# Kernel tuning notes

Measured on AMD Instinct MI355X. Metric: run time of the kernel, lower is better.

Reference implementation:

```python
import jax, jax.numpy as jnp
import numpy as np

V = 50000      # vocab size
FEAT = 300     # glove dim
HID = 512      # num_hidden
C = 20         # class_num (GAT feature width)
L = 2          # num_layers
NH = 4         # num_heads
K = 3          # diffusion hops
ALPHA = 0.1    # teleport prob
N = 76800      # total nodes in batched graph
E = 1250000    # total edges
B = 512        # number of graphs (docs)
SLOPE = 0.2    # leaky relu slope (DGL GAT default)


def setup_inputs() -> dict:
    key = jax.random.key(0)
    ks = jax.random.split(key, 12)
    node_ids = jax.random.randint(ks[0], (N,), 0, V)
    edge_src = jax.random.randint(ks[1], (E,), 0, N)
    edge_dst = jax.random.randint(ks[2], (E,), 0, N)
    graph_ids = jnp.sort(jax.random.randint(ks[3], (N,), 0, B))
    emb = jax.random.uniform(ks[4], (V, FEAT), minval=-0.1, maxval=0.1, dtype=jnp.float32)
    W1 = jax.random.normal(ks[5], (FEAT, HID), dtype=jnp.float32) / np.sqrt(FEAT)
    b1 = jnp.zeros((HID,), jnp.float32)
    W2 = jax.random.normal(ks[6], (HID, C), dtype=jnp.float32) / np.sqrt(HID)
    b2 = jnp.zeros((C,), jnp.float32)
    gat_W = jax.random.normal(ks[7], (L, NH, C, C), dtype=jnp.float32) / np.sqrt(C)
    gat_asrc = jax.random.normal(ks[8], (L, NH, C), dtype=jnp.float32) * 0.1
    gat_adst = jax.random.normal(ks[9], (L, NH, C), dtype=jnp.float32) * 0.1
    ws_W = jax.random.normal(ks[10], (C, 1), dtype=jnp.float32) / np.sqrt(C)
    ws_b = jnp.zeros((1,), jnp.float32)
    return {"node_ids": node_ids, "edge_src": edge_src, "edge_dst": edge_dst,
            "graph_ids": graph_ids, "emb": emb, "W1": W1, "b1": b1, "W2": W2,
            "b2": b2, "gat_W": gat_W, "gat_asrc": gat_asrc, "gat_adst": gat_adst,
            "ws_W": ws_W, "ws_b": ws_b}


def _segment_softmax(e, dst, n):
    # e: [NH, E] edge scores; softmax over edges sharing the same destination node
    seg_max = jax.vmap(lambda v: jax.ops.segment_max(v, dst, num_segments=n))(e)
    seg_max = jnp.where(jnp.isfinite(seg_max), seg_max, 0.0)
    ex = jnp.exp(e - seg_max[:, dst])
    denom = jax.vmap(lambda v: jax.ops.segment_sum(v, dst, num_segments=n))(ex)
    return ex / (denom[:, dst] + 1e-9)


def _forward(node_ids, edge_src, edge_dst, graph_ids, emb, W1, b1, W2, b2,
             gat_W, gat_asrc, gat_adst, ws_W, ws_b):
    x = jnp.take(emb, node_ids, axis=0)              # [N, FEAT] embedding lookup
    x = jax.nn.relu(x @ W1 + b1)                     # [N, HID]
    h = x @ W2 + b2                                  # [N, C]
    for l in range(L):
        z = jnp.einsum('nc,hcd->hnd', h, gat_W[l])   # [NH, N, C]
        es = jnp.einsum('hnd,hd->hn', z, gat_asrc[l])
        ed = jnp.einsum('hnd,hd->hn', z, gat_adst[l])
        e = jax.nn.leaky_relu(es[:, edge_src] + ed[:, edge_dst], SLOPE)  # [NH, E]
        att = _segment_softmax(e, edge_dst, N)       # [NH, E]
        # attention diffusion: H <- (1-alpha) * A_att @ H + alpha * H0
        H0 = z
        Hc = z
        for _ in range(K):
            msg = att[:, :, None] * Hc[:, edge_src, :]                     # [NH, E, C]
            agg = jax.vmap(lambda m: jax.ops.segment_sum(m, edge_dst, num_segments=N))(msg)
            Hc = (1.0 - ALPHA) * agg + ALPHA * H0
        h = Hc.mean(axis=0)                          # merge='mean' over heads
        if l < L - 1:
            h = jax.nn.elu(h)
    gate = jax.nn.sigmoid(h @ ws_W + ws_b)           # [N, 1] WeightAndSum gate
    return jax.ops.segment_sum(h * gate, graph_ids, num_segments=B)  # [B, C]


def reference(node_ids, edge_src, edge_dst, graph_ids, emb, W1, b1, W2, b2,
              gat_W, gat_asrc, gat_adst, ws_W, ws_b):
    return _forward(node_ids, edge_src, edge_dst, graph_ids, emb, W1, b1, W2, b2,
                    gat_W, gat_asrc, gat_adst, ws_W, ws_b)
```

## Files before the change

### kernel.cpp

```cpp
#include <hip/hip_runtime.h>
#include <hip/hip_bf16.h>
#include <hip/hip_fp16.h>
#include <math.h>

#define VOCAB 50000
#define FEAT 300
#define KPAD 320
#define HID 512
#define C 20
#define NL 2
#define NH 4
#define KHOP 3
#define ALPHA 0.1f
#define NNODE 76800
#define NEDGE 1250000
#define NB 512
#define SLOPE 0.2f

#define NBKT 300
#define BKTCAP 5120
#define NSLOT (NBKT * BKTCAP)
#define EPB 5120
#define NEBLK ((NEDGE + EPB - 1) / EPB)

#define BM 32
#define VPAD 50048
#define SX_STRIDE 520
#define HP 24

typedef float f32x4 __attribute__((ext_vector_type(4)));
typedef short bf16x8 __attribute__((ext_vector_type(8)));

__device__ inline unsigned short f2b(float x) {
  __hip_bfloat16 h = __float2bfloat16(x);
  return *reinterpret_cast<unsigned short*>(&h);
}

union U48 {
  uint4 u[3];
  __half2 h[12];
};
__device__ inline U48 ldrow16(const __half* p) {
  U48 r;
  const uint4* q = (const uint4*)p;
  r.u[0] = q[0]; r.u[1] = q[1]; r.u[2] = q[2];
  return r;
}

#define H2SWZ(v, pat) ({ union { __half2 h; int i; } _u; _u.h = (v);          \
                         _u.i = __builtin_amdgcn_ds_swizzle(_u.i, (pat));     \
                         _u.h; })
#define FSWZ(x, pat) __int_as_float(                                          \
    __builtin_amdgcn_ds_swizzle(__float_as_int(x), (pat)))
#define SLOTRED_H2(v) do {                                                    \
    v = __hadd2(v, H2SWZ(v, 0x101F));                                         \
    v = __hadd2(v, H2SWZ(v, 0x201F));                                         \
    v = __hadd2(v, H2SWZ(v, 0x401F)); } while (0)

__global__ void k_cvt_w1(const float* __restrict__ W1, ushort* __restrict__ W1t)
{
  int idx = blockIdx.x * 256 + threadIdx.x;
  int kc = idx >> 12;
  int rem = idx & 4095;
  int col = rem >> 3;
  int j = rem & 7;
  int k = kc * 8 + j;
  W1t[idx] = (k < FEAT) ? f2b(W1[(size_t)k * HID + col]) : (ushort)0;
}

__global__ void k_prep_coef(const float* __restrict__ gatW0,
                            const float* __restrict__ as0,
                            const float* __restrict__ ad0,
                            const float* __restrict__ b2,
                            float* __restrict__ coef, float* __restrict__ bb)
{
  int col = threadIdx.x;
  if (col >= 96) return;
  float cf[C];
  if (col < 80) {
    int hd = col / C, d = col - hd * C;
#pragma unroll
    for (int j = 0; j < C; j++) cf[j] = gatW0[(hd * C + j) * C + d];
  } else if (col < 88) {
    int hd = col - 80;
#pragma unroll
    for (int j = 0; j < C; j++) {
      float s = 0.f;
#pragma unroll
      for (int d = 0; d < C; d++) s += gatW0[(hd * C + j) * C + d] * as0[hd * C + d];
      cf[j] = s;
    }
  } else {
    int hd = col - 88;
#pragma unroll
    for (int j = 0; j < C; j++) {
      float s = 0.f;
#pragma unroll
      for (int d = 0; d < C; d++) s += gatW0[(hd * C + j) * C + d] * ad0[hd * C + d];
      cf[j] = s;
    }
  }
  float bbv = 0.f;
#pragma unroll
  for (int j = 0; j < C; j++) { coef[col * C + j] = cf[j]; bbv += b2[j] * cf[j]; }
  bb[col] = bbv;
}

__global__ void k_prep_wcp(const float* __restrict__ W2,
                           const float* __restrict__ coef,
                           ushort* __restrict__ Wcpt)
{
  int idx = blockIdx.x * 256 + threadIdx.x;
  int kc = idx / 768;
  int rem = idx - kc * 768;
  int col = rem >> 3;
  int j = rem & 7;
  int k = kc * 8 + j;
  float s = 0.f;
#pragma unroll
  for (int jj = 0; jj < C; jj++) s += W2[(size_t)k * C + jj] * coef[col * C + jj];
  Wcpt[idx] = f2b(s);
}

__global__ __launch_bounds__(512, 6) void k_mlp_mfma(
    const float* __restrict__ emb, const ushort* __restrict__ W1t,
    const float* __restrict__ b1, const ushort* __restrict__ Wcpt,
    const float* __restrict__ bb, __half* __restrict__ zfull,
    float* __restrict__ esf, float* __restrict__ edf)
{
  __shared__ ushort smem[16640];
  ushort* sA = smem;
  ushort* sX = smem;

  const int t = threadIdx.x;
  const int lane = t & 63;
  const int w = t >> 6;
  const int v0 = blockIdx.x * BM;
  const int l15 = lane & 15;
  const int l4 = lane >> 4;
  const int cb = w * 64;

#pragma unroll
  for (int j = 0; j < 3; j++) {
    int chunk = j * 512 + t;
    if (chunk < 1280) {
      int row = chunk & 31;
      int kc = chunk >> 5;
      int vr = v0 + row;
      if (vr >= VOCAB) vr = VOCAB - 1;
      int k0 = kc * 8;
      const float* p = emb + (size_t)vr * FEAT + k0;
      ushort u[8];
      if (k0 + 8 <= FEAT) {
        float4 x = *(const float4*)p;
        float4 y = *(const float4*)(p + 4);
        u[0] = f2b(x.x); u[1] = f2b(x.y); u[2] = f2b(x.z); u[3] = f2b(x.w);
        u[4] = f2b(y.x); u[5] = f2b(y.y); u[6] = f2b(y.z); u[7] = f2b(y.w);
      } else {
#pragma unroll
        for (int q = 0; q < 8; q++)
          u[q] = (k0 + q < FEAT) ? f2b(p[q]) : (ushort)0;
      }
      *(uint4*)(sA + (size_t)chunk * 8) = *(const uint4*)u;
    }
  }
  __syncthreads();

  f32x4 acc[2][4];
#pragma unroll
  for (int rt = 0; rt < 2; rt++)
#pragma unroll
    for (int ct = 0; ct < 4; ct++) acc[rt][ct] = (f32x4)0.f;

  for (int ks = 0; ks < 10; ks++) {
    const int kcb = ks * 4 + l4;
    bf16x8 a0 = *(const bf16x8*)(sA + ((size_t)kcb * 32 + l15) * 8);
    bf16x8 a1 = *(const bf16x8*)(sA + ((size_t)kcb * 32 + 16 + l15) * 8);
    const ushort* wb = W1t + ((size_t)kcb * 512 + cb + l15) * 8;
    bf16x8 bf[4];
#pragma unroll
    for (int ct = 0; ct < 4; ct++) bf[ct] = *(const bf16x8*)(wb + ct * 128);
#pragma unroll
    for (int ct = 0; ct < 4; ct++) {
      acc[0][ct] = __builtin_amdgcn_mfma_f32_16x16x32_bf16(a0, bf[ct], acc[0][ct], 0, 0, 0);
      acc[1][ct] = __builtin_amdgcn_mfma_f32_16x16x32_bf16(a1, bf[ct], acc[1][ct], 0, 0, 0);
    }
  }
  __syncthreads();

#pragma unroll
  for (int rt = 0; rt < 2; rt++)
#pragma unroll
    for (int ct = 0; ct < 4; ct++) {
      int col = cb + ct * 16 + l15;
      float bias = b1[col];
#pragma unroll
      for (int r4 = 0; r4 < 4; r4++) {
        int row = rt * 16 + l4 * 4 + r4;
        float x = fmaxf(acc[rt][ct][r4] + bias, 0.f);
        sX[(size_t)row * SX_STRIDE + col] = f2b(x);
      }
    }
  __syncthreads();

  const int ntile = (w < 4) ? 2 : 1;
  for (int i = 0; i < ntile; i++) {
    const int tt = (i == 0) ? w : 8 + w;
    const int rt = tt & 1, ct = tt >> 1;
    const ushort* xb = sX + (size_t)(rt * 16 + l15) * SX_STRIDE + l4 * 8;
    const ushort* wbp = Wcpt + ((size_t)l4 * 96 + ct * 16 + l15) * 8;
    bf16x8 bv[16];
#pragma unroll
    for (int ks = 0; ks < 16; ks++)
      bv[ks] = *(const bf16x8*)(wbp + (size_t)ks * 3072);
    f32x4 a2 = (f32x4)0.f;
#pragma unroll
    for (int ks = 0; ks < 16; ks++) {
      bf16x8 av = *(const bf16x8*)(xb + ks * 32);
      a2 = __builtin_amdgcn_mfma_f32_16x16x32_bf16(av, bv[ks], a2, 0, 0, 0);
    }
    const int col = ct * 16 + l15;
    const float bias = bb[col];
#pragma unroll
    for (int r = 0; r < 4; r++) {
      const int vrow = v0 + rt * 16 + l4 * 4 + r;
      if (vrow >= VOCAB) continue;
      float val = a2[r] + bias;
      if (col < 80) {
        int hd = col / C, c = col - hd * C;
        zfull[((size_t)vrow * NH + hd) * HP + c] = __float2half_rn(val);
      } else if (col < 88) {
        esf[(size_t)vrow * NH + (col - 80)] = val;
      } else {
        edf[(size_t)vrow * NH + (col - 88)] = val;
      }
    }
  }
}

__global__ __launch_bounds__(256) void k_bkt_scatter(
    const int* __restrict__ src, const int* __restrict__ dst,
    int* __restrict__ gcur, int* __restrict__ gbuf)
{
  __shared__ int hist[NBKT];
  __shared__ int lcur[NBKT];
  const int t = threadIdx.x;
  for (int i = t; i < NBKT; i += 256) hist[i] = 0;
  __syncthreads();
  const int base = blockIdx.x * EPB;
#pragma unroll
  for (int j = 0; j < 20; j++) {
    int e = base + j * 256 + t;
    if (e < NEDGE) atomicAdd(&hist[dst[e] >> 8], 1);
  }
  __syncthreads();
  for (int i = t; i < NBKT; i += 256) {
    int v = hist[i];
    lcur[i] = v ? atomicAdd(&gcur[i], v) : 0;
  }
  __syncthreads();
#pragma unroll
  for (int j = 0; j < 20; j++) {
    int e = base + j * 256 + t;
    if (e < NEDGE) {
      int d = dst[e];
      int b = d >> 8;
      int idx = atomicAdd(&lcur[b], 1);
      if (idx < BKTCAP)
        gbuf[(size_t)b * BKTCAP + idx] = (src[e] << 8) | (d & 255);
    }
  }
}

__global__ __launch_bounds__(256) void k_csr_build(
    const int* __restrict__ gcur, const int* __restrict__ gbuf,
    const int* __restrict__ node_ids, int* __restrict__ offs,
    int* __restrict__ deg, int* __restrict__ srcc, int* __restrict__ srcv)
{
  __shared__ int shist[256];
  __shared__ int lcur[256];
  __shared__ int wsum[4];
  const int b = blockIdx.x;
  const int t = threadIdx.x;
  const int base = b * BKTCAP;
  int nb = gcur[b];
  if (nb > BKTCAP) nb = BKTCAP;
  shist[t] = 0;
  __syncthreads();
  for (int i = t; i < nb; i += 256)
    atomicAdd(&shist[gbuf[base + i] & 255], 1);
  __syncthreads();
  int v = shist[t];
  int x = v;
#pragma unroll
  for (int off = 1; off < 64; off <<= 1) {
    int y = __shfl_up(x, off, 64);
    if ((t & 63) >= off) x += y;
  }
  if ((t & 63) == 63) wsum[t >> 6] = x;
  __syncthreads();
  int waveoff = 0;
#pragma unroll
  for (int w = 0; w < 4; w++) waveoff += (w < (t >> 6)) ? wsum[w] : 0;
  int pre = base + waveoff + x - v;
  offs[b * 256 + t] = pre;
  deg[b * 256 + t] = v;
  lcur[t] = pre;
  __syncthreads();
  for (int i = t; i < nb; i += 256) {
    int p = gbuf[base + i];
    int slot = atomicAdd(&lcur[p & 255], 1);
    int s = p >> 8;
    srcc[slot] = s;
    srcv[slot] = node_ids[s];
  }
}

__global__ __launch_bounds__(256) void k_gat_proj(
    const __half* __restrict__ hb, const float* __restrict__ gatW,
    const float* __restrict__ asrc, const float* __restrict__ adst,
    __half* __restrict__ zb, float* __restrict__ es, float* __restrict__ ed)
{
  __shared__ float sW[NH * C * C];
  __shared__ float sa[NH * C], sd[NH * C];
  const int t = threadIdx.x;
  for (int i = t; i < NH * C * C; i += 256) sW[i] = gatW[i];
  if (t < NH * C) { sa[t] = asrc[t]; sd[t] = adst[t]; }
  __syncthreads();
  const int g = blockIdx.x * 256 + t;
  const int head = g & 3;
  const int n = g >> 2;
  U48 hrow = ldrow16(hb + (size_t)n * HP);
  float hr[C];
#pragma unroll
  for (int q = 0; q < 10; q++) {
    float2 f = __half22float2(hrow.h[q]);
    hr[2 * q] = f.x; hr[2 * q + 1] = f.y;
  }
  const float* Wh = &sW[head * C * C];
  const float* ah = &sa[head * C];
  const float* dh = &sd[head * C];
  float zr[C];
  float esv = 0.f, edv = 0.f;
#pragma unroll
  for (int d = 0; d < C; d++) {
    float zv = 0.f;
#pragma unroll
    for (int c = 0; c < C; c++) zv += hr[c] * Wh[c * C + d];
    zr[d] = zv;
    esv += zv * ah[d];
    edv += zv * dh[d];
  }
  U48 o;
#pragma unroll
  for (int q = 0; q < 10; q++)
    o.h[q] = __floats2half2_rn(zr[2 * q], zr[2 * q + 1]);
  o.h[10] = __floats2half2_rn(0.f, 0.f);
  o.h[11] = o.h[10];
  uint4* zo = (uint4*)(zb + (size_t)g * HP);
  zo[0] = o.u[0]; zo[1] = o.u[1]; zo[2] = o.u[2];
  es[g] = esv;
  ed[g] = edv;
}

__global__ __launch_bounds__(256) void k_hop_first(
    const int* __restrict__ offs, const int* __restrict__ deg,
    const int* __restrict__ sidx,
    const float* __restrict__ esT, const float* __restrict__ edT,
    const int* __restrict__ ids, const __half* __restrict__ Zt,
    __half* __restrict__ att, float* __restrict__ invden,
    __half* __restrict__ Hout)
{
  const int t = threadIdx.x;
  const int head = t & 3;
  const int eslot = (t >> 2) & 7;
  const int n = blockIdx.x * 8 + (t >> 5);
  const int g = n * NH + head;
  const int idn = ids ? ids[n] : n;
  const int beg = offs[n], end = beg + deg[n];
  const float edv = edT[(size_t)idn * NH + head];
  __half2 agg[10];
#pragma unroll
  for (int q = 0; q < 10; q++) agg[q] = __floats2half2_rn(0.f, 0.f);
  float den = 0.f;
  int p = beg + eslot;
  while (p + 8 < end) {
    int sv0 = sidx[p];
    int sv1 = sidx[p + 8];
    float es0 = esT[(size_t)sv0 * NH + head];
    float es1 = esT[(size_t)sv1 * NH + head];
    U48 r0 = ldrow16(Zt + ((size_t)sv0 * NH + head) * HP);
    U48 r1 = ldrow16(Zt + ((size_t)sv1 * NH + head) * HP);
    float e0 = es0 + edv; e0 = e0 > 0.f ? e0 : SLOPE * e0;
    float e1 = es1 + edv; e1 = e1 > 0.f ? e1 : SLOPE * e1;
    float ex0 = __expf(e0), ex1 = __expf(e1);
    att[(size_t)p * NH + head] = __float2half_rn(ex0);
    att[(size_t)(p + 8) * NH + head] = __float2half_rn(ex1);
    den += ex0 + ex1;
    __half2 a0 = __float2half2_rn(ex0);
    __half2 a1 = __float2half2_rn(ex1);
#pragma unroll
    for (int q = 0; q < 10; q++) {
      agg[q] = __hfma2(a0, r0.h[q], agg[q]);
      agg[q] = __hfma2(a1, r1.h[q], agg[q]);
    }
    p += 16;
  }
  if (p < end) {
    int sv0 = sidx[p];
    float es0 = esT[(size_t)sv0 * NH + head];
    U48 r0 = ldrow16(Zt + ((size_t)sv0 * NH + head) * HP);
    float e0 = es0 + edv; e0 = e0 > 0.f ? e0 : SLOPE * e0;
    float ex0 = __expf(e0);
    att[(size_t)p * NH + head] = __float2half_rn(ex0);
    den += ex0;
    __half2 a0 = __float2half2_rn(ex0);
#pragma unroll
    for (int q = 0; q < 10; q++) agg[q] = __hfma2(a0, r0.h[q], agg[q]);
  }
#pragma unroll
  for (int q = 0; q < 10; q++) SLOTRED_H2(agg[q]);
  den += FSWZ(den, 0x101F);
  den += FSWZ(den, 0x201F);
  den += FSWZ(den, 0x401F);
  if (eslot == 0) {
    float inv = 1.f / (den + 1e-9f);
    invden[g] = inv;
    U48 h0 = ldrow16(Zt + ((size_t)idn * NH + head) * HP);
    __half2 s2 = __float2half2_rn(inv * (1.0f - ALPHA));
    __half2 al = __float2half2_rn(ALPHA);
    U48 o;
#pragma unroll
    for (int q = 0; q < 10; q++)
      o.h[q] = __hfma2(s2, agg[q], __hmul2(al, h0.h[q]));
    o.h[10] = __floats2half2_rn(0.f, 0.f);
    o.h[11] = o.h[10];
    uint4* op = (uint4*)(Hout + (size_t)g * HP);
    op[0] = o.u[0]; op[1] = o.u[1]; op[2] = o.u[2];
  }
}

__global__ __launch_bounds__(256) void k_hop_mid(
    const int* __restrict__ offs, const int* __restrict__ deg,
    const int* __restrict__ srcc,
    const __half* __restrict__ att, const float* __restrict__ invden,
    const __half* __restrict__ Hin, const __half* __restrict__ Zt,
    const int* __restrict__ ids, __half* __restrict__ Hout)
{
  const int t = threadIdx.x;
  const int head = t & 3;
  const int eslot = (t >> 2) & 7;
  const int n = blockIdx.x * 8 + (t >> 5);
  const int g = n * NH + head;
  const int idn = ids ? ids[n] : n;
  const int beg = offs[n], end = beg + deg[n];
  __half2 agg[10];
#pragma unroll
  for (int q = 0; q < 10; q++) agg[q] = __floats2half2_rn(0.f, 0.f);
  int p = beg + eslot;
  while (p + 8 < end) {
    __half a0h = att[(size_t)p * NH + head];
    __half a1h = att[(size_t)(p + 8) * NH + head];
    int sn0 = srcc[p];
    int sn1 = srcc[p + 8];
    U48 r0 = ldrow16(Hin + ((size_t)sn0 * NH + head) * HP);
    U48 r1 = ldrow16(Hin + ((size_t)sn1 * NH + head) * HP);
    __half2 a0 = __half2half2(a0h);
    __half2 a1 = __half2half2(a1h);
#pragma unroll
    for (int q = 0; q < 10; q++) {
      agg[q] = __hfma2(a0, r0.h[q], agg[q]);
      agg[q] = __hfma2(a1, r1.h[q], agg[q]);
    }
    p += 16;
  }
  if (p < end) {
    __half a0h = att[(size_t)p * NH + head];
    int sn0 = srcc[p];
    U48 r0 = ldrow16(Hin + ((size_t)sn0 * NH + head) * HP);
    __half2 a0 = __half2half2(a0h);
#pragma unroll
    for (int q = 0; q < 10; q++) agg[q] = __hfma2(a0, r0.h[q], agg[q]);
  }
#pragma unroll
  for (int q = 0; q < 10; q++) SLOTRED_H2(agg[q]);
  if (eslot == 0) {
    U48 h0 = ldrow16(Zt + ((size_t)idn * NH + head) * HP);
    __half2 s2 = __float2half2_rn(invden[g] * (1.0f - ALPHA));
    __half2 al = __float2half2_rn(ALPHA);
    U48 o;
#pragma unroll
    for (int q = 0; q < 10; q++)
      o.h[q] = __hfma2(s2, agg[q], __hmul2(al, h0.h[q]));
    o.h[10] = __floats2half2_rn(0.f, 0.f);
    o.h[11] = o.h[10];
    uint4* op = (uint4*)(Hout + (size_t)g * HP);
    op[0] = o.u[0]; op[1] = o.u[1]; op[2] = o.u[2];
  }
}

__global__ __launch_bounds__(256) void k_hop_last_mid(
    const int* __restrict__ offs, const int* __restrict__ deg,
    const int* __restrict__ srcc,
    const __half* __restrict__ att, const float* __restrict__ invden,
    const __half* __restrict__ Hin, const __half* __restrict__ Zt,
    const int* __restrict__ ids, __half* __restrict__ hb)
{
  const int t = threadIdx.x;
  const int head = t & 3;
  const int eslot = (t >> 2) & 7;
  const int n = blockIdx.x * 8 + (t >> 5);
  const int g = n * NH + head;
  const int idn = ids ? ids[n] : n;
  const int beg = offs[n], end = beg + deg[n];
  __half2 agg[10];
#pragma unroll
  for (int q = 0; q < 10; q++) agg[q] = __floats2half2_rn(0.f, 0.f);
  int p = beg + eslot;
  while (p + 8 < end) {
    __half a0h = att[(size_t)p * NH + head];
    __half a1h = att[(size_t)(p + 8) * NH + head];
    int sn0 = srcc[p];
    int sn1 = srcc[p + 8];
    U48 r0 = ldrow16(Hin + ((size_t)sn0 * NH + head) * HP);
    U48 r1 = ldrow16(Hin + ((size_t)sn1 * NH + head) * HP);
    __half2 a0 = __half2half2(a0h);
    __half2 a1 = __half2half2(a1h);
#pragma unroll
    for (int q = 0; q < 10; q++) {
      agg[q] = __hfma2(a0, r0.h[q], agg[q]);
      agg[q] = __hfma2(a1, r1.h[q], agg[q]);
    }
    p += 16;
  }
  if (p < end) {
    __half a0h = att[(size_t)p * NH + head];
    int sn0 = srcc[p];
    U48 r0 = ldrow16(Hin + ((size_t)sn0 * NH + head) * HP);
    __half2 a0 = __half2half2(a0h);
#pragma unroll
    for (int q = 0; q < 10; q++) agg[q] = __hfma2(a0, r0.h[q], agg[q]);
  }
#pragma unroll
  for (int q = 0; q < 10; q++) SLOTRED_H2(agg[q]);
  if (eslot == 0) {
    U48 h0 = ldrow16(Zt + ((size_t)idn * NH + head) * HP);
    __half2 s2 = __float2half2_rn(invden[g] * (1.0f - ALPHA));
    __half2 al = __float2half2_rn(ALPHA);
    float o[C];
#pragma unroll
    for (int q = 0; q < 10; q++) {
      __half2 m = __hfma2(s2, agg[q], __hmul2(al, h0.h[q]));
      m = __hadd2(m, H2SWZ(m, 0x041F));
      m = __hadd2(m, H2SWZ(m, 0x081F));
      float2 f = __half22float2(m);
      o[2 * q]     = f.x * 0.25f;
      o[2 * q + 1] = f.y * 0.25f;
    }
#pragma unroll
    for (int j = 0; j < 5; j++) {
      int c = head * 5 + j;
      float v = o[c];
      v = v > 0.f ? v : __expf(v) - 1.f;
      hb[(size_t)n * HP + c] = __float2half_rn(v);
    }
  }
}

#define RSPAN 16
__global__ __launch_bounds__(256) void k_hop_last_final(
    const int* __restrict__ offs, const int* __restrict__ deg,
    const int* __restrict__ srcc,
    const __half* __restrict__ att, const float* __restrict__ invden,
    const __half* __restrict__ Hin, const __half* __restrict__ Zt,
    const int* __restrict__ gids, const float* __restrict__ wsW,
    const float* __restrict__ wsb, float* __restrict__ out)
{
  __shared__ float sacc[RSPAN * C];
  __shared__ int sgmin;
  const int t = threadIdx.x;
  const int head = t & 3;
  const int eslot = (t >> 2) & 7;
  const int n = blockIdx.x * 8 + (t >> 5);
  const int g = n * NH + head;
  const int beg = offs[n], end = beg + deg[n];
  for (int i = t; i < RSPAN * C; i += 256) sacc[i] = 0.f;
  if (t == 0) sgmin = gids[blockIdx.x * 8];
  __syncthreads();
  __half2 agg[10];
#pragma unroll
  for (int q = 0; q < 10; q++) agg[q] = __floats2half2_rn(0.f, 0.f);
  int p = beg + eslot;
  while (p + 8 < end) {
    __half a0h = att[(size_t)p * NH + head];
    __half a1h = att[(size_t)(p + 8) * NH + head];
    int sn0 = srcc[p];
    int sn1 = srcc[p + 8];
    U48 r0 = ldrow16(Hin + ((size_t)sn0 * NH + head) * HP);
    U48 r1 = ldrow16(Hin + ((size_t)sn1 * NH + head) * HP);
    __half2 a0 = __half2half2(a0h);
    __half2 a1 = __half2half2(a1h);
#pragma unroll
    for (int q = 0; q < 10; q++) {
      agg[q] = __hfma2(a0, r0.h[q], agg[q]);
      agg[q] = __hfma2(a1, r1.h[q], agg[q]);
    }
    p += 16;
  }
  if (p < end) {
    __half a0h = att[(size_t)p * NH + head];
    int sn0 = srcc[p];
    U48 r0 = ldrow16(Hin + ((size_t)sn0 * NH + head) * HP);
    __half2 a0 = __half2half2(a0h);
#pragma unroll
    for (int q = 0; q < 10; q++) agg[q] = __hfma2(a0, r0.h[q], agg[q]);
  }
#pragma unroll
  for (int q = 0; q < 10; q++) SLOTRED_H2(agg[q]);
  if (eslot == 0) {
    U48 h0 = ldrow16(Zt + ((size_t)n * NH + head) * HP);
    __half2 s2 = __float2half2_rn(invden[g] * (1.0f - ALPHA));
    __half2 al = __float2half2_rn(ALPHA);
    float o[C];
#pragma unroll
    for (int q = 0; q < 10; q++) {
      __half2 m = __hfma2(s2, agg[q], __hmul2(al, h0.h[q]));
      m = __hadd2(m, H2SWZ(m, 0x041F));
      m = __hadd2(m, H2SWZ(m, 0x081F));
      float2 f = __half22float2(m);
      o[2 * q]     = f.x * 0.25f;
      o[2 * q + 1] = f.y * 0.25f;
    }
    float dotp = 0.f;
#pragma unroll
    for (int j = 0; j < 5; j++) {
      int c = head * 5 + j;
      dotp += o[c] * wsW[c];
    }
    dotp += FSWZ(dotp, 0x041F);
    dotp += FSWZ(dotp, 0x081F);
    const float gate = 1.f / (1.f + __expf(-(dotp + wsb[0])));
    const int b = gids[n];
    const int lb = b - sgmin;
    if (lb < RSPAN) {
#pragma unroll
      for (int j = 0; j < 5; j++) {
        int c = head * 5 + j;
        atomicAdd(&sacc[lb * C + c], o[c] * gate);
      }
    } else {
#pragma unroll
      for (int j = 0; j < 5; j++) {
        int c = head * 5 + j;
        atomicAdd(&out[(size_t)b * C + c], o[c] * gate);
      }
    }
  }
  __syncthreads();
  for (int i = t; i < RSPAN * C; i += 256) {
    float v = sacc[i];
    if (v != 0.f) atomicAdd(&out[(size_t)(sgmin + i / C) * C + (i - (i / C) * C)], v);
  }
}

extern "C" void kernel_launch(void* const* d_in, const int* in_sizes, int n_in,
                              void* d_out, int out_size, void* d_ws, size_t ws_size,
                              hipStream_t stream)
{
  const int*   node_ids = (const int*)  d_in[0];
  const int*   edge_src = (const int*)  d_in[1];
  const int*   edge_dst = (const int*)  d_in[2];
  const int*   graph_ids= (const int*)  d_in[3];
  const float* emb      = (const float*)d_in[4];
  const float* W1       = (const float*)d_in[5];
  const float* b1       = (const float*)d_in[6];
  const float* W2       = (const float*)d_in[7];
  const float* b2       = (const float*)d_in[8];
  const float* gat_W    = (const float*)d_in[9];
  const float* gat_asrc = (const float*)d_in[10];
  const float* gat_adst = (const float*)d_in[11];
  const float* ws_W     = (const float*)d_in[12];
  const float* ws_b     = (const float*)d_in[13];
  float* out = (float*)d_out;

  float* esf    = (float*)d_ws;
  float* edf    = esf   + (size_t)VPAD * NH;
  float* es     = edf   + (size_t)VPAD * NH;
  float* ed     = es    + (size_t)NNODE * NH;
  float* invden = ed    + (size_t)NNODE * NH;
  float* bb     = invden+ (size_t)NNODE * NH;
  float* coef   = bb + 96;
  int*   offs   = (int*)(coef + 96 * C);
  int*   deg    = offs + NNODE;
  int*   gcur   = deg + NNODE;
  int*   srcc   = gcur + NBKT;
  int*   srcv   = srcc + NSLOT;
  uintptr_t a16 = ((uintptr_t)(srcv + NSLOT) + 15) & ~(uintptr_t)15;
  __half* h_bf  = (__half*)a16;
  __half* zfull = h_bf + (size_t)NNODE * HP;
  __half* zb    = zfull + (size_t)VPAD * NH * HP;
  __half* bufA  = zb    + (size_t)NNODE * NH * HP;
  __half* bufB  = bufA  + (size_t)NNODE * NH * HP;
  ushort* W1t   = (ushort*)(bufB + (size_t)NNODE * NH * HP);
  ushort* Wcpt  = W1t + (size_t)40 * 512 * 8;
  uintptr_t x16 = ((uintptr_t)(Wcpt + 64 * 96 * 8) + 15) & ~(uintptr_t)15;
  int*    gbuf  = (int*)x16;
  __half* att   = (__half*)x16;

  hipMemsetAsync(out, 0, (size_t)NB * C * sizeof(float), stream);
  hipMemsetAsync(gcur, 0, NBKT * sizeof(int), stream);

  k_cvt_w1<<<(40 * 512 * 8) / 256, 256, 0, stream>>>(W1, W1t);
  k_prep_coef<<<1, 128, 0, stream>>>(gat_W, gat_asrc, gat_adst, b2, coef, bb);
  k_prep_wcp<<<(64 * 96 * 8) / 256, 256, 0, stream>>>(W2, coef, Wcpt);

  k_bkt_scatter<<<NEBLK, 256, 0, stream>>>(edge_src, edge_dst, gcur, gbuf);
  k_csr_build<<<NBKT, 256, 0, stream>>>(gcur, gbuf, node_ids,
                                        offs, deg, srcc, srcv);

  k_mlp_mfma<<<VPAD / BM, 512, 0, stream>>>(emb, W1t, b1, Wcpt, bb,
                                            zfull, esf, edf);

  const int HB = NNODE / 8;
  k_hop_first<<<HB, 256, 0, stream>>>(offs, deg, srcv, esf, edf, node_ids,
                                      zfull, att, invden, bufA);
  k_hop_mid<<<HB, 256, 0, stream>>>(offs, deg, srcc, att, invden, bufA, zfull,
                                    node_ids, bufB);
  k_hop_last_mid<<<HB, 256, 0, stream>>>(offs, deg, srcc, att, invden, bufB,
                                         zfull, node_ids, h_bf);
  const int GB = (NH * NNODE) / 256;
  k_gat_proj<<<GB, 256, 0, stream>>>(h_bf, gat_W + (size_t)NH * C * C,
                                     gat_asrc + NH * C, gat_adst + NH * C,
                                     zb, es, ed);
  k_hop_first<<<HB, 256, 0, stream>>>(offs, deg, srcc, es, ed,
                                      (const int*)nullptr, zb, att, invden,
                                      bufA);
  k_hop_mid<<<HB, 256, 0, stream>>>(offs, deg, srcc, att, invden, bufA, zb,
                                    (const int*)nullptr, bufB);
  k_hop_last_final<<<HB, 256, 0, stream>>>(offs, deg, srcc, att, invden, bufB,
                                           zb, graph_ids, ws_W, ws_b, out);
}
```

Before: 442.9 us.

## Fuse layer-2 GAT projection into last hop and shrink feature rows to 20 halves

The separate GAT projection kernel for layer 2 is folded into the last hop of layer 1. Each of the 8 edge slots computes a subset of the 20 output columns using the shared-memory weights, and the attention dot products are reduced with swizzles. This drops a kernel launch and the round trip of the intermediate h buffer. Feature rows are also repacked from a 24-half padded stride to 20 halves, cutting gather bytes in every hop at the cost of 8-byte-aligned loads instead of three 16-byte loads.

```diff
diff --git a/kernel.cpp b/kernel.cpp
--- a/kernel.cpp
+++ b/kernel.cpp
@@ -26,7 +26,6 @@
 #define BM 32
 #define VPAD 50048
 #define SX_STRIDE 520
-#define HP 24
 
 typedef float f32x4 __attribute__((ext_vector_type(4)));
 typedef short bf16x8 __attribute__((ext_vector_type(8)));
@@ -36,15 +35,21 @@
   return *reinterpret_cast<unsigned short*>(&h);
 }
 
-union U48 {
-  uint4 u[3];
-  __half2 h[12];
+union R20 {
+  struct { uint4 a, b; uint2 c; } v;
+  __half2 h[10];
 };
-__device__ inline U48 ldrow16(const __half* p) {
-  U48 r;
-  const uint4* q = (const uint4*)p;
-  r.u[0] = q[0]; r.u[1] = q[1]; r.u[2] = q[2];
+__device__ inline R20 ldrow20(const __half* p) {
+  R20 r;
+  r.v.a = *(const uint4*)p;
+  r.v.b = *(const uint4*)(p + 8);
+  r.v.c = *(const uint2*)(p + 16);
   return r;
+}
+__device__ inline void strow20(__half* p, const R20& r) {
+  *(uint4*)p = r.v.a;
+  *(uint4*)(p + 8) = r.v.b;
+  *(uint2*)(p + 16) = r.v.c;
 }
 
 #define H2SWZ(v, pat) ({ union { __half2 h; int i; } _u; _u.h = (v);          \
@@ -228,7 +233,7 @@
       float val = a2[r] + bias;
       if (col < 80) {
         int hd = col / C, c = col - hd * C;
-        zfull[((size_t)vrow * NH + hd) * HP + c] = __float2half_rn(val);
+        zfull[((size_t)vrow * NH + hd) * 20 + c] = __float2half_rn(val);
       } else if (col < 88) {
         esf[(size_t)vrow * NH + (col - 80)] = val;
       } else {
@@ -316,53 +321,6 @@
   }
 }
 
-__global__ __launch_bounds__(256) void k_gat_proj(
-    const __half* __restrict__ hb, const float* __restrict__ gatW,
-    const float* __restrict__ asrc, const float* __restrict__ adst,
-    __half* __restrict__ zb, float* __restrict__ es, float* __restrict__ ed)
-{
-  __shared__ float sW[NH * C * C];
-  __shared__ float sa[NH * C], sd[NH * C];
-  const int t = threadIdx.x;
-  for (int i = t; i < NH * C * C; i += 256) sW[i] = gatW[i];
-  if (t < NH * C) { sa[t] = asrc[t]; sd[t] = adst[t]; }
-  __syncthreads();
-  const int g = blockIdx.x * 256 + t;
-  const int head = g & 3;
-  const int n = g >> 2;
-  U48 hrow = ldrow16(hb + (size_t)n * HP);
-  float hr[C];
-#pragma unroll
-  for (int q = 0; q < 10; q++) {
-    float2 f = __half22float2(hrow.h[q]);
-    hr[2 * q] = f.x; hr[2 * q + 1] = f.y;
-  }
-  const float* Wh = &sW[head * C * C];
-  const float* ah = &sa[head * C];
-  const float* dh = &sd[head * C];
-  float zr[C];
-  float esv = 0.f, edv = 0.f;
-#pragma unroll
-  for (int d = 0; d < C; d++) {
-    float zv = 0.f;
-#pragma unroll
-    for (int c = 0; c < C; c++) zv += hr[c] * Wh[c * C + d];
-    zr[d] = zv;
-    esv += zv * ah[d];
-    edv += zv * dh[d];
-  }
-  U48 o;
-#pragma unroll
-  for (int q = 0; q < 10; q++)
-    o.h[q] = __floats2half2_rn(zr[2 * q], zr[2 * q + 1]);
-  o.h[10] = __floats2half2_rn(0.f, 0.f);
-  o.h[11] = o.h[10];
-  uint4* zo = (uint4*)(zb + (size_t)g * HP);
-  zo[0] = o.u[0]; zo[1] = o.u[1]; zo[2] = o.u[2];
-  es[g] = esv;
-  ed[g] = edv;
-}
-
 __global__ __launch_bounds__(256) void k_hop_first(
     const int* __restrict__ offs, const int* __restrict__ deg,
     const int* __restrict__ sidx,
@@ -389,8 +347,8 @@
     int sv1 = sidx[p + 8];
     float es0 = esT[(size_t)sv0 * NH + head];
     float es1 = esT[(size_t)sv1 * NH + head];
-    U48 r0 = ldrow16(Zt + ((size_t)sv0 * NH + head) * HP);
-    U48 r1 = ldrow16(Zt + ((size_t)sv1 * NH + head) * HP);
+    R20 r0 = ldrow20(Zt + ((size_t)sv0 * NH + head) * 20);
+    R20 r1 = ldrow20(Zt + ((size_t)sv1 * NH + head) * 20);
     float e0 = es0 + edv; e0 = e0 > 0.f ? e0 : SLOPE * e0;
     float e1 = es1 + edv; e1 = e1 > 0.f ? e1 : SLOPE * e1;
     float ex0 = __expf(e0), ex1 = __expf(e1);
@@ -409,7 +367,7 @@
   if (p < end) {
     int sv0 = sidx[p];
     float es0 = esT[(size_t)sv0 * NH + head];
-    U48 r0 = ldrow16(Zt + ((size_t)sv0 * NH + head) * HP);
+    R20 r0 = ldrow20(Zt + ((size_t)sv0 * NH + head) * 20);
     float e0 = es0 + edv; e0 = e0 > 0.f ? e0 : SLOPE * e0;
     float ex0 = __expf(e0);
     att[(size_t)p * NH + head] = __float2half_rn(ex0);
@@ -426,17 +384,14 @@
   if (eslot == 0) {
     float inv = 1.f / (den + 1e-9f);
     invden[g] = inv;
-    U48 h0 = ldrow16(Zt + ((size_t)idn * NH + head) * HP);
+    R20 h0 = ldrow20(Zt + ((size_t)idn * NH + head) * 20);
     __half2 s2 = __float2half2_rn(inv * (1.0f - ALPHA));
     __half2 al = __float2half2_rn(ALPHA);
-    U48 o;
+    R20 o;
 #pragma unroll
     for (int q = 0; q < 10; q++)
       o.h[q] = __hfma2(s2, agg[q], __hmul2(al, h0.h[q]));
-    o.h[10] = __floats2half2_rn(0.f, 0.f);
-    o.h[11] = o.h[10];
-    uint4* op = (uint4*)(Hout + (size_t)g * HP);
-    op[0] = o.u[0]; op[1] = o.u[1]; op[2] = o.u[2];
+    strow20(Hout + (size_t)g * 20, o);
   }
 }
 
@@ -463,8 +418,8 @@
     __half a1h = att[(size_t)(p + 8) * NH + head];
     int sn0 = srcc[p];
     int sn1 = srcc[p + 8];
-    U48 r0 = ldrow16(Hin + ((size_t)sn0 * NH + head) * HP);
-    U48 r1 = ldrow16(Hin + ((size_t)sn1 * NH + head) * HP);
+    R20 r0 = ldrow20(Hin + ((size_t)sn0 * NH + head) * 20);
+    R20 r1 = ldrow20(Hin + ((size_t)sn1 * NH + head) * 20);
     __half2 a0 = __half2half2(a0h);
     __half2 a1 = __half2half2(a1h);
 #pragma unroll
@@ -477,7 +432,7 @@
   if (p < end) {
     __half a0h = att[(size_t)p * NH + head];
     int sn0 = srcc[p];
-    U48 r0 = ldrow16(Hin + ((size_t)sn0 * NH + head) * HP);
+    R20 r0 = ldrow20(Hin + ((size_t)sn0 * NH + head) * 20);
     __half2 a0 = __half2half2(a0h);
 #pragma unroll
     for (int q = 0; q < 10; q++) agg[q] = __hfma2(a0, r0.h[q], agg[q]);
@@ -485,28 +440,34 @@
 #pragma unroll
   for (int q = 0; q < 10; q++) SLOTRED_H2(agg[q]);
   if (eslot == 0) {
-    U48 h0 = ldrow16(Zt + ((size_t)idn * NH + head) * HP);
+    R20 h0 = ldrow20(Zt + ((size_t)idn * NH + head) * 20);
     __half2 s2 = __float2half2_rn(invden[g] * (1.0f - ALPHA));
     __half2 al = __float2half2_rn(ALPHA);
-    U48 o;
+    R20 o;
 #pragma unroll
     for (int q = 0; q < 10; q++)
       o.h[q] = __hfma2(s2, agg[q], __hmul2(al, h0.h[q]));
-    o.h[10] = __floats2half2_rn(0.f, 0.f);
-    o.h[11] = o.h[10];
-    uint4* op = (uint4*)(Hout + (size_t)g * HP);
-    op[0] = o.u[0]; op[1] = o.u[1]; op[2] = o.u[2];
-  }
-}
-
-__global__ __launch_bounds__(256) void k_hop_last_mid(
+    strow20(Hout + (size_t)g * 20, o);
+  }
+}
+
+__global__ __launch_bounds__(256) void k_hop_last_proj(
     const int* __restrict__ offs, const int* __restrict__ deg,
     const int* __restrict__ srcc,
     const __half* __restrict__ att, const float* __restrict__ invden,
     const __half* __restrict__ Hin, const __half* __restrict__ Zt,
-    const int* __restrict__ ids, __half* __restrict__ hb)
-{
+    const int* __restrict__ ids,
+    const float* __restrict__ gatW1, const float* __restrict__ as1,
+    const float* __restrict__ ad1,
+    __half* __restrict__ zb, float* __restrict__ es, float* __restrict__ ed)
+{
+  __shared__ float sW[NH * C * C];
+  __shared__ float sa[NH * C], sd[NH * C];
   const int t = threadIdx.x;
+  for (int i = t; i < NH * C * C; i += 256) sW[i] = gatW1[i];
+  if (t < NH * C) { sa[t] = as1[t]; sd[t] = ad1[t]; }
+  __syncthreads();
+
   const int head = t & 3;
   const int eslot = (t >> 2) & 7;
   const int n = blockIdx.x * 8 + (t >> 5);
@@ -522,8 +483,8 @@
     __half a1h = att[(size_t)(p + 8) * NH + head];
     int sn0 = srcc[p];
     int sn1 = srcc[p + 8];
-    U48 r0 = ldrow16(Hin + ((size_t)sn0 * NH + head) * HP);
-    U48 r1 = ldrow16(Hin + ((size_t)sn1 * NH + head) * HP);
+    R20 r0 = ldrow20(Hin + ((size_t)sn0 * NH + head) * 20);
+    R20 r1 = ldrow20(Hin + ((size_t)sn1 * NH + head) * 20);
     __half2 a0 = __half2half2(a0h);
     __half2 a1 = __half2half2(a1h);
 #pragma unroll
@@ -536,34 +497,52 @@
   if (p < end) {
     __half a0h = att[(size_t)p * NH + head];
     int sn0 = srcc[p];
-    U48 r0 = ldrow16(Hin + ((size_t)sn0 * NH + head) * HP);
+    R20 r0 = ldrow20(Hin + ((size_t)sn0 * NH + head) * 20);
     __half2 a0 = __half2half2(a0h);
 #pragma unroll
     for (int q = 0; q < 10; q++) agg[q] = __hfma2(a0, r0.h[q], agg[q]);
   }
 #pragma unroll
   for (int q = 0; q < 10; q++) SLOTRED_H2(agg[q]);
+
+  R20 h0 = ldrow20(Zt + ((size_t)idn * NH + head) * 20);
+  __half2 s2 = __float2half2_rn(invden[g] * (1.0f - ALPHA));
+  __half2 al = __float2half2_rn(ALPHA);
+  float o[C];
+#pragma unroll
+  for (int q = 0; q < 10; q++) {
+    __half2 m = __hfma2(s2, agg[q], __hmul2(al, h0.h[q]));
+    m = __hadd2(m, H2SWZ(m, 0x041F));
+    m = __hadd2(m, H2SWZ(m, 0x081F));
+    float2 f = __half22float2(m);
+    float v0 = f.x * 0.25f, v1 = f.y * 0.25f;
+    o[2 * q]     = v0 > 0.f ? v0 : __expf(v0) - 1.f;
+    o[2 * q + 1] = v1 > 0.f ? v1 : __expf(v1) - 1.f;
+  }
+
+  const float* Wh = &sW[head * C * C];
+  float esp = 0.f, edp = 0.f;
+#pragma unroll
+  for (int j = 0; j < 3; j++) {
+    int d = eslot + j * 8;
+    if (d < C) {
+      float zv = 0.f;
+#pragma unroll
+      for (int c = 0; c < C; c++) zv += o[c] * Wh[c * C + d];
+      esp += zv * sa[head * C + d];
+      edp += zv * sd[head * C + d];
+      zb[((size_t)n * NH + head) * 20 + d] = __float2half_rn(zv);
+    }
+  }
+  esp += FSWZ(esp, 0x101F);
+  esp += FSWZ(esp, 0x201F);
+  esp += FSWZ(esp, 0x401F);
+  edp += FSWZ(edp, 0x101F);
+  edp += FSWZ(edp, 0x201F);
+  edp += FSWZ(edp, 0x401F);
   if (eslot == 0) {
-    U48 h0 = ldrow16(Zt + ((size_t)idn * NH + head) * HP);
-    __half2 s2 = __float2half2_rn(invden[g] * (1.0f - ALPHA));
-    __half2 al = __float2half2_rn(ALPHA);
-    float o[C];
-#pragma unroll
-    for (int q = 0; q < 10; q++) {
-      __half2 m = __hfma2(s2, agg[q], __hmul2(al, h0.h[q]));
-      m = __hadd2(m, H2SWZ(m, 0x041F));
-      m = __hadd2(m, H2SWZ(m, 0x081F));
-      float2 f = __half22float2(m);
-      o[2 * q]     = f.x * 0.25f;
-      o[2 * q + 1] = f.y * 0.25f;
-    }
-#pragma unroll
-    for (int j = 0; j < 5; j++) {
-      int c = head * 5 + j;
-      float v = o[c];
-      v = v > 0.f ? v : __expf(v) - 1.f;
-      hb[(size_t)n * HP + c] = __float2half_rn(v);
-    }
+    es[g] = esp;
+    ed[g] = edp;
   }
 }
 
@@ -596,8 +575,8 @@
     __half a1h = att[(size_t)(p + 8) * NH + head];
     int sn0 = srcc[p];
     int sn1 = srcc[p + 8];
-    U48 r0 = ldrow16(Hin + ((size_t)sn0 * NH + head) * HP);
-    U48 r1 = ldrow16(Hin + ((size_t)sn1 * NH + head) * HP);
+    R20 r0 = ldrow20(Hin + ((size_t)sn0 * NH + head) * 20);
+    R20 r1 = ldrow20(Hin + ((size_t)sn1 * NH + head) * 20);
     __half2 a0 = __half2half2(a0h);
     __half2 a1 = __half2half2(a1h);
 #pragma unroll
@@ -610,7 +589,7 @@
   if (p < end) {
     __half a0h = att[(size_t)p * NH + head];
     int sn0 = srcc[p];
-    U48 r0 = ldrow16(Hin + ((size_t)sn0 * NH + head) * HP);
+    R20 r0 = ldrow20(Hin + ((size_t)sn0 * NH + head) * 20);
     __half2 a0 = __half2half2(a0h);
 #pragma unroll
     for (int q = 0; q < 10; q++) agg[q] = __hfma2(a0, r0.h[q], agg[q]);
@@ -618,7 +597,7 @@
 #pragma unroll
   for (int q = 0; q < 10; q++) SLOTRED_H2(agg[q]);
   if (eslot == 0) {
-    U48 h0 = ldrow16(Zt + ((size_t)n * NH + head) * HP);
+    R20 h0 = ldrow20(Zt + ((size_t)n * NH + head) * 20);
     __half2 s2 = __float2half2_rn(invden[g] * (1.0f - ALPHA));
     __half2 al = __float2half2_rn(ALPHA);
     float o[C];
@@ -696,12 +675,11 @@
   int*   srcc   = gcur + NBKT;
   int*   srcv   = srcc + NSLOT;
   uintptr_t a16 = ((uintptr_t)(srcv + NSLOT) + 15) & ~(uintptr_t)15;
-  __half* h_bf  = (__half*)a16;
-  __half* zfull = h_bf + (size_t)NNODE * HP;
-  __half* zb    = zfull + (size_t)VPAD * NH * HP;
-  __half* bufA  = zb    + (size_t)NNODE * NH * HP;
-  __half* bufB  = bufA  + (size_t)NNODE * NH * HP;
-  ushort* W1t   = (ushort*)(bufB + (size_t)NNODE * NH * HP);
+  __half* zfull = (__half*)a16;
+  __half* zb    = zfull + (size_t)VPAD * NH * 20;
+  __half* bufA  = zb    + (size_t)NNODE * NH * 20;
+  __half* bufB  = bufA  + (size_t)NNODE * NH * 20;
+  ushort* W1t   = (ushort*)(bufB + (size_t)NNODE * NH * 20);
   ushort* Wcpt  = W1t + (size_t)40 * 512 * 8;
   uintptr_t x16 = ((uintptr_t)(Wcpt + 64 * 96 * 8) + 15) & ~(uintptr_t)15;
   int*    gbuf  = (int*)x16;
@@ -726,12 +704,11 @@
                                       zfull, att, invden, bufA);
   k_hop_mid<<<HB, 256, 0, stream>>>(offs, deg, srcc, att, invden, bufA, zfull,
                                     node_ids, bufB);
-  k_hop_last_mid<<<HB, 256, 0, stream>>>(offs, deg, srcc, att, invden, bufB,
-                                         zfull, node_ids, h_bf);
-  const int GB = (NH * NNODE) / 256;
-  k_gat_proj<<<GB, 256, 0, stream>>>(h_bf, gat_W + (size_t)NH * C * C,
-                                     gat_asrc + NH * C, gat_adst + NH * C,
-                                     zb, es, ed);
+  k_hop_last_proj<<<HB, 256, 0, stream>>>(offs, deg, srcc, att, invden, bufB,
+                                          zfull, node_ids,
+                                          gat_W + (size_t)NH * C * C,
+                                          gat_asrc + NH * C, gat_adst + NH * C,
+                                          zb, es, ed);
   k_hop_first<<<HB, 256, 0, stream>>>(offs, deg, srcc, es, ed,
                                       (const int*)nullptr, zb, att, invden,
                                       bufA);
```

Result: faster. 402.7 us (-9.1%).
